# Kernel optimization log

Measured on AMD Instinct MI355X. Metric: run time of the kernel, lower is better.

## Reference

```python
import jax, jax.numpy as jnp
import numpy as np
import math

B, T, C = 8, 2048, 1024
H = 16
HD = C // H  # 64 head dim; RoPE operates on HD//2 complex pairs


def setup_inputs() -> dict:
    key = jax.random.key(0)
    k1, k2, k3, k4 = jax.random.split(key, 4)
    x = jax.random.normal(k1, (B, T, C), dtype=jnp.float32)
    # RoPE angles theta[t, i] = t * base**(-2i/HD), as in standard precompute_freqs_cis
    inv_freq = 1.0 / (10000.0 ** (jnp.arange(0, HD, 2, dtype=jnp.float32) / HD))
    freqs = jnp.arange(T, dtype=jnp.float32)[:, None] * inv_freq[None, :]  # [T, HD//2]
    W_attn = jax.random.normal(k2, (C, 3 * C), dtype=jnp.float32) * 0.02
    b_attn = jnp.zeros((3 * C,), dtype=jnp.float32)
    W_proj = jax.random.normal(k3, (C, C), dtype=jnp.float32) * 0.02
    b_proj = jnp.zeros((C,), dtype=jnp.float32)
    return {"x": x, "freqs": freqs, "W_attn": W_attn, "b_attn": b_attn,
            "W_proj": W_proj, "b_proj": b_proj}


def _apply_rope(t, cos, sin):
    # t: [B, T, H, HD] -> view as complex pairs on last dim
    tr = t.reshape(*t.shape[:-1], HD // 2, 2)
    t0, t1 = tr[..., 0], tr[..., 1]
    out0 = t0 * cos - t1 * sin
    out1 = t0 * sin + t1 * cos
    return jnp.stack([out0, out1], axis=-1).reshape(t.shape)


def reference(x, freqs, W_attn, b_attn, W_proj, b_proj):
    Bx, Tx, Cx = x.shape
    qkv = x @ W_attn + b_attn                      # [B, T, 3C]
    q, k, v = jnp.split(qkv, 3, axis=2)
    q = q.reshape(Bx, Tx, H, HD)
    k = k.reshape(Bx, Tx, H, HD)
    v = v.reshape(Bx, Tx, H, HD)
    # rotary embedding (freqs broadcast over batch and heads)
    cos = jnp.cos(freqs)[None, :, None, :]        # [1, T, 1, HD//2]
    sin = jnp.sin(freqs)[None, :, None, :]
    q = _apply_rope(q, cos, sin)
    k = _apply_rope(k, cos, sin)
    # [B, H, T, HD]
    q = q.transpose(0, 2, 1, 3)
    k = k.transpose(0, 2, 1, 3)
    v = v.transpose(0, 2, 1, 3)
    scale = 1.0 / math.sqrt(HD)
    scores = jnp.einsum('bhqd,bhkd->bhqk', q, k) * scale
    causal = jnp.tril(jnp.ones((Tx, Tx), dtype=bool))
    scores = jnp.where(causal[None, None], scores, jnp.finfo(scores.dtype).min)
    att = jax.nn.softmax(scores, axis=-1)
    y = jnp.einsum('bhqk,bhkd->bhqd', att, v)     # [B, H, T, HD]
    y = y.transpose(0, 2, 1, 3).reshape(Bx, Tx, Cx)
    y = y @ W_proj + b_proj
    return y
```

## Files before the change

kernel.cpp:

```cpp
#include <hip/hip_runtime.h>

#define B_ 8
#define T_ 2048
#define C_ 1024
#define H_ 16
#define HD_ 64
#define BH_ (B_ * H_)
#define M_ (B_ * T_)

typedef __attribute__((ext_vector_type(8))) short short8;
typedef __attribute__((ext_vector_type(4))) float floatx4;
typedef __attribute__((ext_vector_type(16))) float floatx16;

__device__ __forceinline__ short f2bf(float f) {
  unsigned int u = __float_as_uint(f);
  u += 0x7fffu + ((u >> 16) & 1u);
  return (short)(u >> 16);
}

__device__ __forceinline__ unsigned cvtpk(float a, float b) {
  unsigned r;
  asm("v_cvt_pk_bf16_f32 %0, %1, %2" : "=v"(r) : "v"(a), "v"(b));
  return r;
}

__device__ __forceinline__ float ex2(float x) {
  float r;
  asm("v_exp_f32 %0, %1" : "=v"(r) : "v"(x));
  return r;
}

__device__ __forceinline__ void g2lds16(const void* g, void* l) {
  __builtin_amdgcn_global_load_lds(
      (const __attribute__((address_space(1))) unsigned int*)g,
      (__attribute__((address_space(3))) unsigned int*)l, 16, 0, 0);
}

__global__ void cvt_x_kernel(const float* __restrict__ x, short* __restrict__ xb, int n8) {
  int i = blockIdx.x * 256 + threadIdx.x;
  if (i >= n8) return;
  const float4* p = reinterpret_cast<const float4*>(x) + (size_t)i * 2;
  float4 a = p[0], b = p[1];
  short8 o;
  o[0] = f2bf(a.x); o[1] = f2bf(a.y); o[2] = f2bf(a.z); o[3] = f2bf(a.w);
  o[4] = f2bf(b.x); o[5] = f2bf(b.y); o[6] = f2bf(b.z); o[7] = f2bf(b.w);
  reinterpret_cast<short8*>(xb)[i] = o;
}

__global__ void transpose_w_kernel(const float* __restrict__ W, short* __restrict__ Wt,
                                   int K, int N) {
  __shared__ float tile[64][65];
  const int k0 = blockIdx.y * 64;
  const int n0 = blockIdx.x * 64;
  const int tid = threadIdx.x;
  const int cc = tid & 15, rr = tid >> 4;
#pragma unroll
  for (int p = 0; p < 4; ++p) {
    int r = p * 16 + rr;
    float4 v = *reinterpret_cast<const float4*>(&W[(size_t)(k0 + r) * N + n0 + cc * 4]);
    tile[r][cc * 4 + 0] = v.x; tile[r][cc * 4 + 1] = v.y;
    tile[r][cc * 4 + 2] = v.z; tile[r][cc * 4 + 3] = v.w;
  }
  __syncthreads();
  const int kk8 = tid & 7, nn = tid >> 3;
#pragma unroll
  for (int p = 0; p < 2; ++p) {
    int n = p * 32 + nn;
    short8 o;
#pragma unroll
    for (int j = 0; j < 8; ++j) o[j] = f2bf(tile[kk8 * 8 + j][n]);
    *reinterpret_cast<short8*>(&Wt[(size_t)(n0 + n) * K + k0 + kk8 * 8]) = o;
  }
}

__global__ void trig_kernel(const float* __restrict__ freqs, float2* __restrict__ cs, int n) {
  int i = blockIdx.x * 256 + threadIdx.x;
  if (i < n) {
    float f = freqs[i];
    cs[i] = make_float2(cosf(f), sinf(f));
  }
}

#define WAIT8 asm volatile("s_waitcnt vmcnt(8)" ::: "memory")
#define WAIT6 asm volatile("s_waitcnt vmcnt(6)" ::: "memory")
#define WAIT4 asm volatile("s_waitcnt vmcnt(4)" ::: "memory")
#define WAIT3 asm volatile("s_waitcnt vmcnt(3)" ::: "memory")
#define WAIT2 asm volatile("s_waitcnt vmcnt(2)" ::: "memory")
#define WAIT0 asm volatile("s_waitcnt vmcnt(0)" ::: "memory")

#define GITER(T, CUR, NXT)                                                        \
  {                                                                               \
    const int tbR = ((T) & 3) << 15;                                              \
                                     \
    _Pragma("unroll") for (int i = 0; i < 4; ++i)                                 \
        af1[i] = *reinterpret_cast<const short8*>(ldsb + tbR + aoff[4 + i]);      \
    __builtin_amdgcn_s_setprio(1);                                                \
    _Pragma("unroll") for (int m = 0; m < 4; ++m)                                 \
        _Pragma("unroll") for (int n = 0; n < 4; ++n)                             \
            acc[m][n] = __builtin_amdgcn_mfma_f32_16x16x32_bf16(                  \
                af0[m], CUR[n], acc[m][n], 0, 0, 0);                              \
    __builtin_amdgcn_s_setprio(0);                                                \
    \
    if ((T) + 3 < NT) { stageA((T) + 3); stageB((T) + 3); }                       \
    if ((T) < NT - 3) { WAIT8; }                                                  \
    else if ((T) == NT - 3) { WAIT4; }                                            \
    else if ((T) == NT - 2) { WAIT0; }                                            \
    asm volatile("s_waitcnt lgkmcnt(0)" ::: "memory");                            \
    __builtin_amdgcn_s_barrier();                                                 \
    if ((T) + 1 < NT) {                                                           \
      const int tbN = (((T) + 1) & 3) << 15;                                      \
      _Pragma("unroll") for (int n = 0; n < 4; ++n)                               \
          NXT[n] = *reinterpret_cast<const short8*>(ldsb + tbN + boff[n]);        \
      _Pragma("unroll") for (int i = 0; i < 4; ++i)                               \
          af0[i] = *reinterpret_cast<const short8*>(ldsb + tbN + aoff[i]);        \
    }                                                                             \
    __builtin_amdgcn_s_setprio(1);                                                \
    _Pragma("unroll") for (int m = 0; m < 4; ++m)                                 \
        _Pragma("unroll") for (int n = 0; n < 4; ++n)                             \
            acc[4 + m][n] = __builtin_amdgcn_mfma_f32_16x16x32_bf16(              \
                af1[m], CUR[n], acc[4 + m][n], 0, 0, 0);                          \
    __builtin_amdgcn_s_setprio(0);                                                \
  }

__global__ __launch_bounds__(512, 2) void gemm8_kernel(
    const short* __restrict__ A, const short* __restrict__ Bt,
    const float* __restrict__ bias, int Ndim, int nbx,
    short* __restrict__ Qw, short* __restrict__ Kw, short* __restrict__ Vw,
    const float2* __restrict__ trig) {
  constexpr int Kd = 1024, NT = 32;
  __shared__ short lds[65536];
  const char* ldsb = reinterpret_cast<const char*>(lds);
  const int tid = threadIdx.x, l = tid & 63, w = tid >> 6;
  const int wr = w >> 2, wc = w & 3;

  const int nwg = gridDim.x, qq8 = nwg >> 3;
  const int bid = blockIdx.x;
  const int wg = (bid & 7) * qq8 + (bid >> 3);
  const int npx = nbx >> 2;
  const int p = wg >> 4, q = wg & 15;
  const int bx = (p % npx) * 4 + (q & 3);
  const int by = (p / npx) * 4 + (q >> 2);
  const int m0 = by * 256, n0 = bx * 256;

  const int sup1 = tid >> 3;
  const int lcS = (tid & 7) ^ (sup1 & 7);
  const int rowS = 2 * sup1 + (lcS >> 2);
  const int colS = (lcS & 3) << 3;

  const int cl = l & 15, r4h = l >> 4;
  const int supL = cl >> 1;
  const int aslot = (((cl & 1) << 2) + r4h) ^ supL;
  int aoff[8], boff[4];
#pragma unroll
  for (int m = 0; m < 8; ++m)
    aoff[m] = (wr * 64 + m * 8 + supL) * 128 + aslot * 16;
#pragma unroll
  for (int n = 0; n < 4; ++n)
    boff[n] = 16384 + (wc * 32 + n * 8 + supL) * 128 + aslot * 16;

  auto stageA = [&](int t) {
    const int sb = (t & 3) << 15;
    const int k0 = t * 32;
    g2lds16(&A[(size_t)(m0 + rowS) * Kd + k0 + colS], (char*)lds + sb + tid * 16);
    g2lds16(&A[(size_t)(m0 + rowS + 128) * Kd + k0 + colS],
            (char*)lds + sb + 8192 + tid * 16);
  };
  auto stageB = [&](int t) {
    const int sb = ((t & 3) << 15) + 16384;
    const int k0 = t * 32;
    g2lds16(&Bt[(size_t)(n0 + rowS) * Kd + k0 + colS], (char*)lds + sb + tid * 16);
    g2lds16(&Bt[(size_t)(n0 + rowS + 128) * Kd + k0 + colS],
            (char*)lds + sb + 8192 + tid * 16);
  };

  floatx4 acc[8][4] = {};
  short8 af0[4], af1[4], bbA[4], bbB[4];

  stageA(0); stageB(0);
  stageA(1); stageB(1);
  stageA(2); stageB(2);
  WAIT8;
  __builtin_amdgcn_s_barrier();
#pragma unroll
  for (int n = 0; n < 4; ++n)
    bbA[n] = *reinterpret_cast<const short8*>(ldsb + boff[n]);
#pragma unroll
  for (int i = 0; i < 4; ++i)
    af0[i] = *reinterpret_cast<const short8*>(ldsb + aoff[i]);

  for (int t = 0; t < NT; t += 2) {
    GITER(t, bbA, bbB);
    GITER(t + 1, bbB, bbA);
  }

  const int r4 = r4h * 4;
  if (n0 >= 2048) {
    short* vr = &lds[w * 8192];
    const int hh = ((n0 - 2048) >> 6) + wc;
    const int bhv = (m0 >> 11) * 16 + hh;
    const int t0g = (m0 & 2047) + wr * 128;
#pragma unroll
    for (int m = 0; m < 8; ++m) {
#pragma unroll
      for (int n = 0; n < 4; ++n) {
        const int gn = n0 + wc * 64 + n * 16 + cl;
        const float bs = bias[gn];
        const int d = n * 16 + cl;
        const int sW = m * 2 + (r4h >> 1);
        const int byte = d * 256 + (((sW ^ (d & 15))) << 4) + ((r4h & 1) << 3);
        uint2 pv;
        pv.x = cvtpk(acc[m][n][0] + bs, acc[m][n][1] + bs);
        pv.y = cvtpk(acc[m][n][2] + bs, acc[m][n][3] + bs);
        *reinterpret_cast<uint2*>(reinterpret_cast<char*>(vr) + byte) = pv;
      }
    }
#pragma unroll
    for (int g = 0; g < 16; ++g) {
      const int d = g * 4 + r4h;
      const int byte = d * 256 + (((cl ^ (d & 15))) << 4);
      short8 vv = *reinterpret_cast<const short8*>(
          reinterpret_cast<const char*>(vr) + byte);
      *reinterpret_cast<short8*>(&Vw[((size_t)bhv * 64 + d) * 2048 + t0g + cl * 8]) = vv;
    }
  } else {
#pragma unroll
    for (int m = 0; m < 8; ++m) {
#pragma unroll
      for (int n = 0; n < 4; ++n) {
        const int gn = n0 + wc * 64 + n * 16 + cl;
#pragma unroll
        for (int r = 0; r < 4; ++r) {
          const int gm = m0 + wr * 128 + m * 16 + r4 + r;
          float v = acc[m][n][r] + bias[gn];
          const int b = gm >> 11, t = gm & 2047;
          const int ccol = gn & 1023;
          const int h = ccol >> 6, d = ccol & 63;
          const int bh = b * 16 + h;
          float2 cs = trig[t * 32 + (d >> 1)];
          float p2 = __shfl_xor(v, 1);
          float o = (d & 1) ? (p2 * cs.y + v * cs.x) : (v * cs.x - p2 * cs.y);
          if ((gn >> 10) == 0) {
            Qw[((size_t)bh * T_ + t) * HD_ + d] = f2bf(o * 0.18033688011112042f);
          } else {
            Kw[((size_t)bh * T_ + t) * HD_ + d] = f2bf(o);
          }
        }
      }
    }
  }
}

__global__ __launch_bounds__(512, 1) void gemm_proj_kernel(
    const short* __restrict__ A, const short* __restrict__ Bt,
    const float* __restrict__ bias, float* __restrict__ outF) {
  constexpr int Kd = 1024, NT = 32, Nd = 1024;
  __shared__ short lds[49152];
  const char* ldsb = reinterpret_cast<const char*>(lds);
  const int tid = threadIdx.x, l = tid & 63, w = tid >> 6;
  const int wr = w >> 1, wc = w & 1;

  const int nwg = gridDim.x, qq8 = nwg >> 3;
  const int bid = blockIdx.x;
  const int wg = (bid & 7) * qq8 + (bid >> 3);
  const int p = wg >> 4, q = wg & 15;
  const int bx = (p % 2) * 4 + (q & 3);
  const int by = (p / 2) * 4 + (q >> 2);
  const int m0 = by * 256, n0 = bx * 128;

  const int sup1 = tid >> 3;
  const int lcS = (tid & 7) ^ (sup1 & 7);
  const int rowS = 2 * sup1 + (lcS >> 2);
  const int colS = (lcS & 3) << 3;

  const int cl = l & 15, r4h = l >> 4;
  const int supL = cl >> 1;
  const int aslot = (((cl & 1) << 2) + r4h) ^ supL;
  int aoff[4], boff[4];
#pragma unroll
  for (int m = 0; m < 4; ++m)
    aoff[m] = (wr * 32 + m * 8 + supL) * 128 + aslot * 16;
#pragma unroll
  for (int n = 0; n < 4; ++n)
    boff[n] = 16384 + (wc * 32 + n * 8 + supL) * 128 + aslot * 16;

  auto stageA = [&](int t) {
    const int sb = (t & 3) * 24576;
    const int k0 = t * 32;
    g2lds16(&A[(size_t)(m0 + rowS) * Kd + k0 + colS], (char*)lds + sb + tid * 16);
    g2lds16(&A[(size_t)(m0 + rowS + 128) * Kd + k0 + colS],
            (char*)lds + sb + 8192 + tid * 16);
  };
  auto stageB = [&](int t) {
    const int sb = (t & 3) * 24576 + 16384;
    g2lds16(&Bt[(size_t)(n0 + rowS) * Kd + t * 32 + colS],
            (char*)lds + sb + tid * 16);
  };

  floatx4 acc[4][4] = {};
  short8 af0[2], af1[2], bbA[4], bbB[4];

  stageA(0); stageB(0);
  stageA(1); stageB(1);
  stageA(2); stageB(2);
  WAIT6;
  __builtin_amdgcn_s_barrier();
#pragma unroll
  for (int n = 0; n < 4; ++n)
    bbA[n] = *reinterpret_cast<const short8*>(ldsb + boff[n]);
  af0[0] = *reinterpret_cast<const short8*>(ldsb + aoff[0]);
  af0[1] = *reinterpret_cast<const short8*>(ldsb + aoff[1]);

#define PITER(T, CUR, NXT)                                                        \
  {                                                                               \
    const int tbR = ((T) & 3) * 24576;                                            \
    af1[0] = *reinterpret_cast<const short8*>(ldsb + tbR + aoff[2]);              \
    af1[1] = *reinterpret_cast<const short8*>(ldsb + tbR + aoff[3]);              \
    __builtin_amdgcn_s_setprio(1);                                                \
    _Pragma("unroll") for (int m = 0; m < 2; ++m)                                 \
        _Pragma("unroll") for (int n = 0; n < 4; ++n)                             \
            acc[m][n] = __builtin_amdgcn_mfma_f32_16x16x32_bf16(                  \
                af0[m], CUR[n], acc[m][n], 0, 0, 0);                              \
    __builtin_amdgcn_s_setprio(0);                                                \
    if ((T) + 3 < NT) { stageA((T) + 3); stageB((T) + 3); }                       \
    if ((T) < NT - 3) { WAIT6; }                                                  \
    else if ((T) == NT - 3) { WAIT3; }                                            \
    else if ((T) == NT - 2) { WAIT0; }                                            \
    asm volatile("s_waitcnt lgkmcnt(0)" ::: "memory");                            \
    __builtin_amdgcn_s_barrier();                                                 \
    if ((T) + 1 < NT) {                                                           \
      const int tbN = (((T) + 1) & 3) * 24576;                                    \
      _Pragma("unroll") for (int n = 0; n < 4; ++n)                               \
          NXT[n] = *reinterpret_cast<const short8*>(ldsb + tbN + boff[n]);        \
      af0[0] = *reinterpret_cast<const short8*>(ldsb + tbN + aoff[0]);            \
      af0[1] = *reinterpret_cast<const short8*>(ldsb + tbN + aoff[1]);            \
    }                                                                             \
    __builtin_amdgcn_s_setprio(1);                                                \
    _Pragma("unroll") for (int m = 0; m < 2; ++m)                                 \
        _Pragma("unroll") for (int n = 0; n < 4; ++n)                             \
            acc[2 + m][n] = __builtin_amdgcn_mfma_f32_16x16x32_bf16(              \
                af1[m], CUR[n], acc[2 + m][n], 0, 0, 0);                          \
    __builtin_amdgcn_s_setprio(0);                                                \
  }

  for (int t = 0; t < NT; t += 2) {
    PITER(t, bbA, bbB);
    PITER(t + 1, bbB, bbA);
  }
#undef PITER

  const int r4 = r4h * 4;
#pragma unroll
  for (int m = 0; m < 4; ++m) {
#pragma unroll
    for (int n = 0; n < 4; ++n) {
      const int gn = n0 + wc * 64 + n * 16 + cl;
      const float bs = bias[gn];
#pragma unroll
      for (int r = 0; r < 4; ++r) {
        const int gm = m0 + wr * 64 + m * 16 + r4 + r;
        outF[(size_t)gm * Nd + gn] = acc[m][n][r] + bs;
      }
    }
  }
}

__global__ __launch_bounds__(256) void attn_kernel(
    const short* __restrict__ Q, const short* __restrict__ Kw,
    const short* __restrict__ Vt, short* __restrict__ Y) {
  __shared__ short lds[3][8192];
  const int tid = threadIdx.x, l = tid & 63, w = tid >> 6;
  const int ql = l & 31, hi = l >> 5;
  const int bh = blockIdx.x;
  const int qb = 15 - (int)blockIdx.y;
  const int q0w = qb * 128 + w * 32;
  const int jlast = 2 * qb + (w >> 1);
  const int nj = 2 * qb + 2;

  short8 qf[4];
  {
    const size_t qbase = ((size_t)bh * T_ + q0w + ql) * HD_;
#pragma unroll
    for (int s = 0; s < 4; ++s)
      qf[s] = *reinterpret_cast<const short8*>(&Q[qbase + s * 16 + hi * 8]);
  }

  int koffs[4], voffs[4];
#pragma unroll
  for (int s = 0; s < 4; ++s)
    koffs[s] = ql * 64 + (((2 * s + hi) ^ (ql & 7)) * 8);
#pragma unroll
  for (int s2 = 0; s2 < 2; ++s2)
#pragma unroll
    for (int h = 0; h < 2; ++h) {
      int r = 16 * h + (ql >> 1);
      int lc = (ql & 1) * 4 + 2 * s2 + hi;
      voffs[s2 * 2 + h] = r * 64 + ((lc ^ (r & 7)) * 8);
    }

  const int rowSt = tid >> 3, pSt = tid & 7;
  const int gkSt = pSt ^ (rowSt & 7);
  const int dvSt = 2 * rowSt + (gkSt >> 2), kcSt = gkSt & 3;
  const short* kg0 = &Kw[((size_t)bh * T_ + rowSt) * HD_ + gkSt * 8];
  const short* kg1 = &Kw[((size_t)bh * T_ + rowSt + 32) * HD_ + gkSt * 8];
  const short* vg0 = &Vt[((size_t)bh * HD_ + dvSt) * T_ + kcSt * 8];
  const short* vg1 = vg0 + 32;

  floatx16 o0 = {}, o1 = {};
  float l_run = 0.f;

#define STAGE_KV(buf)                                   \
  {                                                     \
    g2lds16(kg0, &lds[buf][0] + tid * 8);               \
    g2lds16(kg1, &lds[buf][2048] + tid * 8);            \
    g2lds16(vg0, &lds[buf][4096] + tid * 8);            \
    g2lds16(vg1, &lds[buf][6144] + tid * 8);            \
    kg0 += 64 * HD_; kg1 += 64 * HD_;                   \
    vg0 += 64; vg1 += 64;                               \
  }

  auto do_half = [&](const short* bK, const short* bV, int koff_add, int vbase,
                     bool domask) {
    floatx16 sx;
#pragma unroll
    for (int r = 0; r < 16; ++r) sx[r] = -16.0f;
#pragma unroll
    for (int s = 0; s < 4; ++s) {
      short8 ka = *reinterpret_cast<const short8*>(bK + koff_add + koffs[s]);
      sx = __builtin_amdgcn_mfma_f32_32x32x16_bf16(ka, qf[s], sx, 0, 0, 0);
    }
    if (domask) {
#pragma unroll
      for (int r = 0; r < 16; ++r) {
        int kb = (r & 3) + 8 * (r >> 2) + 4 * hi;
        if (kb > ql) sx[r] = -1e30f;
      }
    }
#pragma unroll
    for (int r = 0; r < 16; ++r) sx[r] = ex2(sx[r]);
    float a0 = (sx[0] + sx[1]) + (sx[2] + sx[3]);
    float a1 = (sx[4] + sx[5]) + (sx[6] + sx[7]);
    float a2 = (sx[8] + sx[9]) + (sx[10] + sx[11]);
    float a3 = (sx[12] + sx[13]) + (sx[14] + sx[15]);
    l_run += (a0 + a1) + (a2 + a3);
    unsigned pw[8];
#pragma unroll
    for (int i = 0; i < 8; ++i) pw[i] = cvtpk(sx[2 * i], sx[2 * i + 1]);
#pragma unroll
    for (int s2 = 0; s2 < 2; ++s2) {
      unsigned a0w = pw[4 * s2 + 0], a1w = pw[4 * s2 + 1];
      unsigned a2w = pw[4 * s2 + 2], a3w = pw[4 * s2 + 3];
      asm("v_permlane32_swap_b32 %0, %1" : "+v"(a0w), "+v"(a2w));
      asm("v_permlane32_swap_b32 %0, %1" : "+v"(a1w), "+v"(a3w));
      union { unsigned u[4]; short8 s8; } pb;
      pb.u[0] = a0w; pb.u[1] = a1w; pb.u[2] = a2w; pb.u[3] = a3w;
#pragma unroll
      for (int h = 0; h < 2; ++h) {
        short8 va = *reinterpret_cast<const short8*>(bV + vbase + voffs[s2 * 2 + h]);
        if (h == 0) o0 = __builtin_amdgcn_mfma_f32_32x32x16_bf16(va, pb.s8, o0, 0, 0, 0);
        else        o1 = __builtin_amdgcn_mfma_f32_32x32x16_bf16(va, pb.s8, o1, 0, 0, 0);
      }
    }
  };

  STAGE_KV(0);
  STAGE_KV(1);

  for (int j = 0; j < nj; ++j) {
    if (j == nj - 1) { WAIT0; } else { WAIT4; }
    __builtin_amdgcn_s_barrier();
    if (j + 2 < nj) STAGE_KV((j + 2) % 3);

    if (j <= jlast) {
      const short* bK = &lds[j % 3][0];
      const short* bV = &lds[j % 3][4096];
      const bool diag = (j == jlast);
      do_half(bK, bV, 0, 0, diag && ((w & 1) == 0));
      if (!diag || (w & 1))
        do_half(bK, bV, 2048, 2048, diag);
    }
  }

  l_run += __shfl_xor(l_run, 32);
  float inv = 1.0f / l_run;
#pragma unroll
  for (int r = 0; r < 16; ++r) { o0[r] *= inv; o1[r] *= inv; }
  __syncthreads();
  short* tb2 = &lds[0][0] + w * 2048;
#pragma unroll
  for (int h = 0; h < 2; ++h) {
#pragma unroll
    for (int qd = 0; qd < 4; ++qd) {
      int dbase = 32 * h + 8 * qd + 4 * hi;
      uint2 v;
      v.x = h == 0 ? cvtpk(o0[4 * qd], o0[4 * qd + 1]) : cvtpk(o1[4 * qd], o1[4 * qd + 1]);
      v.y = h == 0 ? cvtpk(o0[4 * qd + 2], o0[4 * qd + 3]) : cvtpk(o1[4 * qd + 2], o1[4 * qd + 3]);
      int byte = (ql * 128 + dbase * 2) ^ ((ql & 7) << 4);
      *reinterpret_cast<uint2*>(reinterpret_cast<char*>(tb2) + byte) = v;
    }
  }
  __syncthreads();
  const int bb = bh >> 4, hh = bh & 15;
#pragma unroll
  for (int p = 0; p < 4; ++p) {
    int c = p * 64 + l;
    int q = c >> 3, dc = c & 7;
    int byte = (q * 128 + dc * 16) ^ ((q & 7) << 4);
    short8 v = *reinterpret_cast<const short8*>(reinterpret_cast<const char*>(tb2) + byte);
    *reinterpret_cast<short8*>(
        &Y[((size_t)(bb * T_ + q0w + q)) * C_ + hh * 64 + dc * 8]) = v;
  }
#undef STAGE_KV
}

extern "C" void kernel_launch(void* const* d_in, const int* in_sizes, int n_in,
                              void* d_out, int out_size, void* d_ws, size_t ws_size,
                              hipStream_t stream) {
  const float* x      = (const float*)d_in[0];
  const float* freqs  = (const float*)d_in[1];
  const float* W_attn = (const float*)d_in[2];
  const float* b_attn = (const float*)d_in[3];
  const float* W_proj = (const float*)d_in[4];
  const float* b_proj = (const float*)d_in[5];
  float* out = (float*)d_out;
  char* ws = (char*)d_ws;

  const size_t SZ_QKV = (size_t)BH_ * T_ * HD_ * 2;
  short* Qw  = (short*)(ws);
  short* Kw  = (short*)(ws + SZ_QKV);
  short* Vt  = (short*)(ws + 2 * SZ_QKV);
  short* Xb  = (short*)(ws + 3 * SZ_QKV);
  short* WtA = (short*)(ws + 4 * SZ_QKV);
  short* WtP = (short*)(ws + 4 * SZ_QKV + 6291456);
  float2* trig = (float2*)(ws + 4 * SZ_QKV + 6291456 + 2097152);

  cvt_x_kernel<<<(M_ * C_ / 8 + 255) / 256, 256, 0, stream>>>(x, Xb, M_ * C_ / 8);
  transpose_w_kernel<<<dim3(3 * C_ / 64, C_ / 64), 256, 0, stream>>>(W_attn, WtA, C_, 3 * C_);
  transpose_w_kernel<<<dim3(C_ / 64, C_ / 64), 256, 0, stream>>>(W_proj, WtP, C_, C_);
  trig_kernel<<<(T_ * 32 + 255) / 256, 256, 0, stream>>>(freqs, trig, T_ * 32);

  gemm8_kernel<<<dim3((3 * C_ / 256) * (M_ / 256)), 512, 0, stream>>>(
      Xb, WtA, b_attn, 3 * C_, 3 * C_ / 256, Qw, Kw, Vt, trig);

  attn_kernel<<<dim3(BH_, 16), 256, 0, stream>>>(Qw, Kw, Vt, Xb);

  gemm_proj_kernel<<<dim3((C_ / 128) * (M_ / 256)), 512, 0, stream>>>(
      Xb, WtP, b_proj, out);
}
```

Baseline: 275.1 us.

## Shrink QKV GEMM tile to 128x256 and double the grid

Changes the QKV projection GEMM from 256x256 to 128x256 output tiles, doubling the number of workgroups. LDS staging buffers, fragment counts, wait counts and the V-transpose epilogue swizzle are all reworked to fit the smaller tile, and the launch bound becomes one block per CU. The aim is better load balance across CUs and a smaller per-block footprint. The cost is lower operand reuse per loaded byte and narrower V-store rows.

```diff
diff --git a/kernel.cpp b/kernel.cpp
--- a/kernel.cpp
+++ b/kernel.cpp
@@ -88,47 +88,13 @@
 #define WAIT2 asm volatile("s_waitcnt vmcnt(2)" ::: "memory")
 #define WAIT0 asm volatile("s_waitcnt vmcnt(0)" ::: "memory")
 
-#define GITER(T, CUR, NXT)                                                        \
-  {                                                                               \
-    const int tbR = ((T) & 3) << 15;                                              \
-                                     \
-    _Pragma("unroll") for (int i = 0; i < 4; ++i)                                 \
-        af1[i] = *reinterpret_cast<const short8*>(ldsb + tbR + aoff[4 + i]);      \
-    __builtin_amdgcn_s_setprio(1);                                                \
-    _Pragma("unroll") for (int m = 0; m < 4; ++m)                                 \
-        _Pragma("unroll") for (int n = 0; n < 4; ++n)                             \
-            acc[m][n] = __builtin_amdgcn_mfma_f32_16x16x32_bf16(                  \
-                af0[m], CUR[n], acc[m][n], 0, 0, 0);                              \
-    __builtin_amdgcn_s_setprio(0);                                                \
-    \
-    if ((T) + 3 < NT) { stageA((T) + 3); stageB((T) + 3); }                       \
-    if ((T) < NT - 3) { WAIT8; }                                                  \
-    else if ((T) == NT - 3) { WAIT4; }                                            \
-    else if ((T) == NT - 2) { WAIT0; }                                            \
-    asm volatile("s_waitcnt lgkmcnt(0)" ::: "memory");                            \
-    __builtin_amdgcn_s_barrier();                                                 \
-    if ((T) + 1 < NT) {                                                           \
-      const int tbN = (((T) + 1) & 3) << 15;                                      \
-      _Pragma("unroll") for (int n = 0; n < 4; ++n)                               \
-          NXT[n] = *reinterpret_cast<const short8*>(ldsb + tbN + boff[n]);        \
-      _Pragma("unroll") for (int i = 0; i < 4; ++i)                               \
-          af0[i] = *reinterpret_cast<const short8*>(ldsb + tbN + aoff[i]);        \
-    }                                                                             \
-    __builtin_amdgcn_s_setprio(1);                                                \
-    _Pragma("unroll") for (int m = 0; m < 4; ++m)                                 \
-        _Pragma("unroll") for (int n = 0; n < 4; ++n)                             \
-            acc[4 + m][n] = __builtin_amdgcn_mfma_f32_16x16x32_bf16(              \
-                af1[m], CUR[n], acc[4 + m][n], 0, 0, 0);                          \
-    __builtin_amdgcn_s_setprio(0);                                                \
-  }
-
-__global__ __launch_bounds__(512, 2) void gemm8_kernel(
+__global__ __launch_bounds__(512, 1) void gemm_qkv_kernel(
     const short* __restrict__ A, const short* __restrict__ Bt,
-    const float* __restrict__ bias, int Ndim, int nbx,
+    const float* __restrict__ bias,
     short* __restrict__ Qw, short* __restrict__ Kw, short* __restrict__ Vw,
     const float2* __restrict__ trig) {
-  constexpr int Kd = 1024, NT = 32;
-  __shared__ short lds[65536];
+  constexpr int Kd = 1024, NT = 32, nbx = 12;
+  __shared__ short lds[49152];
   const char* ldsb = reinterpret_cast<const char*>(lds);
   const int tid = threadIdx.x, l = tid & 63, w = tid >> 6;
   const int wr = w >> 2, wc = w & 3;
@@ -140,7 +106,7 @@
   const int p = wg >> 4, q = wg & 15;
   const int bx = (p % npx) * 4 + (q & 3);
   const int by = (p / npx) * 4 + (q >> 2);
-  const int m0 = by * 256, n0 = bx * 256;
+  const int m0 = by * 128, n0 = bx * 256;
 
   const int sup1 = tid >> 3;
   const int lcS = (tid & 7) ^ (sup1 & 7);
@@ -150,87 +116,119 @@
   const int cl = l & 15, r4h = l >> 4;
   const int supL = cl >> 1;
   const int aslot = (((cl & 1) << 2) + r4h) ^ supL;
-  int aoff[8], boff[4];
-#pragma unroll
-  for (int m = 0; m < 8; ++m)
-    aoff[m] = (wr * 64 + m * 8 + supL) * 128 + aslot * 16;
+  int aoff[4], boff[4];
+#pragma unroll
+  for (int m = 0; m < 4; ++m)
+    aoff[m] = (wr * 32 + m * 8 + supL) * 128 + aslot * 16;
 #pragma unroll
   for (int n = 0; n < 4; ++n)
-    boff[n] = 16384 + (wc * 32 + n * 8 + supL) * 128 + aslot * 16;
+    boff[n] = 8192 + (wc * 32 + n * 8 + supL) * 128 + aslot * 16;
 
   auto stageA = [&](int t) {
-    const int sb = (t & 3) << 15;
-    const int k0 = t * 32;
-    g2lds16(&A[(size_t)(m0 + rowS) * Kd + k0 + colS], (char*)lds + sb + tid * 16);
-    g2lds16(&A[(size_t)(m0 + rowS + 128) * Kd + k0 + colS],
-            (char*)lds + sb + 8192 + tid * 16);
+    const int sb = (t & 3) * 24576;
+    g2lds16(&A[(size_t)(m0 + rowS) * Kd + t * 32 + colS],
+            (char*)lds + sb + tid * 16);
   };
   auto stageB = [&](int t) {
-    const int sb = ((t & 3) << 15) + 16384;
+    const int sb = (t & 3) * 24576 + 8192;
     const int k0 = t * 32;
     g2lds16(&Bt[(size_t)(n0 + rowS) * Kd + k0 + colS], (char*)lds + sb + tid * 16);
     g2lds16(&Bt[(size_t)(n0 + rowS + 128) * Kd + k0 + colS],
             (char*)lds + sb + 8192 + tid * 16);
   };
 
-  floatx4 acc[8][4] = {};
-  short8 af0[4], af1[4], bbA[4], bbB[4];
+  floatx4 acc[4][4] = {};
+  short8 af0[2], af1[2], bbA[4], bbB[4];
 
   stageA(0); stageB(0);
   stageA(1); stageB(1);
   stageA(2); stageB(2);
-  WAIT8;
+  WAIT6;
   __builtin_amdgcn_s_barrier();
 #pragma unroll
   for (int n = 0; n < 4; ++n)
     bbA[n] = *reinterpret_cast<const short8*>(ldsb + boff[n]);
-#pragma unroll
-  for (int i = 0; i < 4; ++i)
-    af0[i] = *reinterpret_cast<const short8*>(ldsb + aoff[i]);
+  af0[0] = *reinterpret_cast<const short8*>(ldsb + aoff[0]);
+  af0[1] = *reinterpret_cast<const short8*>(ldsb + aoff[1]);
+
+#define QITER(T, CUR, NXT)                                                        \
+  {                                                                               \
+    const int tbR = ((T) & 3) * 24576;                                            \
+    af1[0] = *reinterpret_cast<const short8*>(ldsb + tbR + aoff[2]);              \
+    af1[1] = *reinterpret_cast<const short8*>(ldsb + tbR + aoff[3]);              \
+    __builtin_amdgcn_s_setprio(1);                                                \
+    _Pragma("unroll") for (int m = 0; m < 2; ++m)                                 \
+        _Pragma("unroll") for (int n = 0; n < 4; ++n)                             \
+            acc[m][n] = __builtin_amdgcn_mfma_f32_16x16x32_bf16(                  \
+                af0[m], CUR[n], acc[m][n], 0, 0, 0);                              \
+    __builtin_amdgcn_s_setprio(0);                                                \
+    if ((T) + 3 < NT) { stageA((T) + 3); stageB((T) + 3); }                       \
+    if ((T) < NT - 3) { WAIT6; }                                                  \
+    else if ((T) == NT - 3) { WAIT3; }                                            \
+    else if ((T) == NT - 2) { WAIT0; }                                            \
+    asm volatile("s_waitcnt lgkmcnt(0)" ::: "memory");                            \
+    __builtin_amdgcn_s_barrier();                                                 \
+    if ((T) + 1 < NT) {                                                           \
+      const int tbN = (((T) + 1) & 3) * 24576;                                    \
+      _Pragma("unroll") for (int n = 0; n < 4; ++n)                               \
+          NXT[n] = *reinterpret_cast<const short8*>(ldsb + tbN + boff[n]);        \
+      af0[0] = *reinterpret_cast<const short8*>(ldsb + tbN + aoff[0]);            \
+      af0[1] = *reinterpret_cast<const short8*>(ldsb + tbN + aoff[1]);            \
+    }                                                                             \
+    __builtin_amdgcn_s_setprio(1);                                                \
+    _Pragma("unroll") for (int m = 0; m < 2; ++m)                                 \
+        _Pragma("unroll") for (int n = 0; n < 4; ++n)                             \
+            acc[2 + m][n] = __builtin_amdgcn_mfma_f32_16x16x32_bf16(              \
+                af1[m], CUR[n], acc[2 + m][n], 0, 0, 0);                          \
+    __builtin_amdgcn_s_setprio(0);                                                \
+  }
 
   for (int t = 0; t < NT; t += 2) {
-    GITER(t, bbA, bbB);
-    GITER(t + 1, bbB, bbA);
-  }
+    QITER(t, bbA, bbB);
+    QITER(t + 1, bbB, bbA);
+  }
+#undef QITER
 
   const int r4 = r4h * 4;
   if (n0 >= 2048) {
-    short* vr = &lds[w * 8192];
+    short* vr = &lds[w * 4096];
     const int hh = ((n0 - 2048) >> 6) + wc;
     const int bhv = (m0 >> 11) * 16 + hh;
-    const int t0g = (m0 & 2047) + wr * 128;
-#pragma unroll
-    for (int m = 0; m < 8; ++m) {
+    const int t0g = (m0 & 2047) + wr * 64;
+#pragma unroll
+    for (int m = 0; m < 4; ++m) {
 #pragma unroll
       for (int n = 0; n < 4; ++n) {
         const int gn = n0 + wc * 64 + n * 16 + cl;
         const float bs = bias[gn];
         const int d = n * 16 + cl;
         const int sW = m * 2 + (r4h >> 1);
-        const int byte = d * 256 + (((sW ^ (d & 15))) << 4) + ((r4h & 1) << 3);
+        const int byte = d * 128 + ((sW ^ (d & 7)) << 4) + ((r4h & 1) << 3);
         uint2 pv;
         pv.x = cvtpk(acc[m][n][0] + bs, acc[m][n][1] + bs);
         pv.y = cvtpk(acc[m][n][2] + bs, acc[m][n][3] + bs);
         *reinterpret_cast<uint2*>(reinterpret_cast<char*>(vr) + byte) = pv;
       }
     }
-#pragma unroll
-    for (int g = 0; g < 16; ++g) {
-      const int d = g * 4 + r4h;
-      const int byte = d * 256 + (((cl ^ (d & 15))) << 4);
+    const int d0 = l >> 3, sl = l & 7;
+#pragma unroll
+    for (int g = 0; g < 8; ++g) {
+      const int d = g * 8 + d0;
+      const int byte = d * 128 + ((sl ^ d0) << 4);
       short8 vv = *reinterpret_cast<const short8*>(
           reinterpret_cast<const char*>(vr) + byte);
-      *reinterpret_cast<short8*>(&Vw[((size_t)bhv * 64 + d) * 2048 + t0g + cl * 8]) = vv;
+      *reinterpret_cast<short8*>(
+          &Vw[((size_t)bhv * 64 + d) * 2048 + t0g + sl * 8]) = vv;
     }
   } else {
 #pragma unroll
-    for (int m = 0; m < 8; ++m) {
+    for (int m = 0; m < 4; ++m) {
 #pragma unroll
       for (int n = 0; n < 4; ++n) {
         const int gn = n0 + wc * 64 + n * 16 + cl;
 #pragma unroll
         for (int r = 0; r < 4; ++r) {
-          const int gm = m0 + wr * 128 + m * 16 + r4 + r;
+          const int gm = m0 + wr * 64 + m * 16 + r4 + r;
           float v = acc[m][n][r] + bias[gn];
           const int b = gm >> 11, t = gm & 2047;
           const int ccol = gn & 1023;
@@ -538,8 +536,8 @@
   transpose_w_kernel<<<dim3(C_ / 64, C_ / 64), 256, 0, stream>>>(W_proj, WtP, C_, C_);
   trig_kernel<<<(T_ * 32 + 255) / 256, 256, 0, stream>>>(freqs, trig, T_ * 32);
 
-  gemm8_kernel<<<dim3((3 * C_ / 256) * (M_ / 256)), 512, 0, stream>>>(
-      Xb, WtA, b_attn, 3 * C_, 3 * C_ / 256, Qw, Kw, Vt, trig);
+  gemm_qkv_kernel<<<dim3((M_ / 128) * (3 * C_ / 256)), 512, 0, stream>>>(
+      Xb, WtA, b_attn, Qw, Kw, Vt, trig);
 
   attn_kernel<<<dim3(BH_, 16), 256, 0, stream>>>(Qw, Kw, Vt, Xb);
 
```

After: 309.4 us. +12.5%, slower.
